# Kernel tuning notes

Measured on AMD Instinct MI355X. Metric: run time of the kernel, lower is better.

## Reference

```python
import jax, jax.numpy as jnp
import numpy as np

ALPHA = 0.2  # LeakyReLU negative slope
NEG_INF = -9e15  # matches torch -9000000000000000.0


def setup_inputs() -> dict:
    key = jax.random.key(0)
    k1, k2, k3, k4, k5, k6 = jax.random.split(key, 6)
    N, F_in, F_out = 4096, 512, 256
    adj = jax.random.randint(k1, (N, N), 0, 2, dtype=jnp.int32)
    h = jax.random.normal(k2, (N, F_in), dtype=jnp.float32)
    # proj: Linear(F_in, F_out)
    W = jax.random.normal(k3, (F_in, F_out), dtype=jnp.float32) * (1.0 / np.sqrt(F_in))
    b = jax.random.normal(k4, (F_out,), dtype=jnp.float32) * 0.01
    # proj_a: Linear(2*F_out, 1) split into the two halves acting on src/dst features
    a1 = jax.random.normal(k5, (F_out,), dtype=jnp.float32) * (1.0 / np.sqrt(2 * F_out))
    a2 = jax.random.normal(k6, (F_out,), dtype=jnp.float32) * (1.0 / np.sqrt(2 * F_out))
    a_b = jnp.zeros((), dtype=jnp.float32)
    return {"adj": adj, "h": h, "W": W, "b": b, "a1": a1, "a2": a2, "a_b": a_b}


def reference(adj, h, W, b, a1, a2, a_b):
    # wh = proj(h): [N, F_out]
    wh = h @ W + b
    # Fused form of the N x N x 2F concat + Linear(2F,1):
    # logits[i, j] = wh[i] . a1 + wh[j] . a2 + a_b
    f_src = wh @ a1  # [N]
    f_dst = wh @ a2  # [N]
    e = jax.nn.leaky_relu(f_src[:, None] + f_dst[None, :] + a_b, negative_slope=ALPHA)
    e = jnp.where(adj > 0, e, NEG_INF)
    att = jax.nn.softmax(e, axis=-1)  # F.softmax legacy dim=1 for 2D
    # dropout: inference mode (no-op) for deterministic reference
    out = att @ wh  # [N, F_out]
    return jax.nn.elu(out)  # concat=True
```

## Files before the change

### kernel.cpp

```cpp
#include <hip/hip_runtime.h>

#define NN   4096
#define FIN  512
#define FOUT 256
#define ALPHA 0.2f

typedef __attribute__((ext_vector_type(8))) short short8;
typedef __attribute__((ext_vector_type(4))) float f32x4;
typedef unsigned short u16;

__device__ __forceinline__ u16 f2bf(float x) {
    union { float f; unsigned u; } v; v.f = x;
    unsigned r = v.u + 0x7FFF + ((v.u >> 16) & 1);
    return (u16)(r >> 16);
}

__global__ __launch_bounds__(256) void k_wt(const float* __restrict__ W,
                                            u16* __restrict__ Wt,
                                            float* __restrict__ fs,
                                            float* __restrict__ fd) {
    __shared__ float s[64 * 65];
    const int t  = threadIdx.x;
    const int g  = (blockIdx.y * gridDim.x + blockIdx.x) * 256 + t;
    if (g < NN) fs[g] = 0.f; else fd[g - NN] = 0.f;
    const int f0 = blockIdx.x * 64;
    const int k0 = blockIdx.y * 64;
    #pragma unroll
    for (int p = 0; p < 4; ++p) {
        int q = t + 256 * p, rr = q >> 4, cc = q & 15;
        float4 w4 = *(const float4*)&W[(size_t)(k0 + rr) * FOUT + f0 + cc * 4];
        s[(cc * 4 + 0) * 65 + rr] = w4.x;
        s[(cc * 4 + 1) * 65 + rr] = w4.y;
        s[(cc * 4 + 2) * 65 + rr] = w4.z;
        s[(cc * 4 + 3) * 65 + rr] = w4.w;
    }
    __syncthreads();
    #pragma unroll
    for (int p = 0; p < 4; ++p) {
        int q = t + 256 * p, f = q >> 4, kg = q & 15;
        ushort4 o;
        o.x = f2bf(s[f * 65 + kg * 4 + 0]);
        o.y = f2bf(s[f * 65 + kg * 4 + 1]);
        o.z = f2bf(s[f * 65 + kg * 4 + 2]);
        o.w = f2bf(s[f * 65 + kg * 4 + 3]);
        *(ushort4*)&Wt[(size_t)(f0 + f) * FIN + k0 + kg * 4] = o;
    }
}

#define HS 520
__global__ __launch_bounds__(256) void k_proj(const float* __restrict__ h,
                                              const u16* __restrict__ Wt,
                                              const float* __restrict__ bias,
                                              const float* __restrict__ a1,
                                              const float* __restrict__ a2,
                                              u16* __restrict__ whT,
                                              float* __restrict__ fs,
                                              float* __restrict__ fd) {
    __shared__ u16 s_h[32 * HS];
    const int t  = threadIdx.x;
    const int f0 = blockIdx.x * 64;
    const int i0 = blockIdx.y * 32;
    #pragma unroll
    for (int p = 0; p < 16; ++p) {
        int q = t + 256 * p, row = q >> 7, c4 = q & 127;
        float4 v = *(const float4*)&h[(size_t)(i0 + row) * FIN + c4 * 4];
        ushort4 o; o.x = f2bf(v.x); o.y = f2bf(v.y); o.z = f2bf(v.z); o.w = f2bf(v.w);
        *(ushort4*)&s_h[row * HS + c4 * 4] = o;
    }
    __syncthreads();
    const int w = t >> 6, l = t & 63, n = l & 15, quad = l >> 4;
    const int hh = w & 1, fh = w >> 1;
    f32x4 acc[2] = {{0.f,0.f,0.f,0.f},{0.f,0.f,0.f,0.f}};
    #pragma unroll
    for (int k0 = 0; k0 < FIN; k0 += 32) {
        short8 a = *(const short8*)&s_h[(hh * 16 + n) * HS + k0 + quad * 8];
        short8 b0 = *(const short8*)&Wt[(size_t)(f0 + fh * 32 + n) * FIN + k0 + quad * 8];
        short8 b1 = *(const short8*)&Wt[(size_t)(f0 + fh * 32 + 16 + n) * FIN + k0 + quad * 8];
        acc[0] = __builtin_amdgcn_mfma_f32_16x16x32_bf16(a, b0, acc[0], 0, 0, 0);
        acc[1] = __builtin_amdgcn_mfma_f32_16x16x32_bf16(a, b1, acc[1], 0, 0, 0);
    }
    const int fb = f0 + fh * 32 + n;
    const float bv0 = bias[fb],  bv1 = bias[fb + 16];
    const float a10 = a1[fb],    a11 = a1[fb + 16];
    const float a20 = a2[fb],    a21 = a2[fb + 16];
    u16* wt_tile = whT + (size_t)(i0 >> 5) * (FOUT * 32);
    float d1[4], d2[4];
    #pragma unroll
    for (int r = 0; r < 4; ++r) {
        const int ic = hh * 16 + quad * 4 + r;
        const float v0 = acc[0][r] + bv0;
        const float v1 = acc[1][r] + bv1;
        wt_tile[fb * 32 + ic]        = f2bf(v0);
        wt_tile[(fb + 16) * 32 + ic] = f2bf(v1);
        d1[r] = v0 * a10 + v1 * a11;
        d2[r] = v0 * a20 + v1 * a21;
    }
    #pragma unroll
    for (int m = 1; m < 16; m <<= 1) {
        #pragma unroll
        for (int r = 0; r < 4; ++r) {
            d1[r] += __shfl_xor(d1[r], m);
            d2[r] += __shfl_xor(d2[r], m);
        }
    }
    if (n == 0) {
        #pragma unroll
        for (int r = 0; r < 4; ++r) {
            const int i = i0 + hh * 16 + quad * 4 + r;
            atomicAdd(&fs[i], d1[r]);
            atomicAdd(&fd[i], d2[r]);
        }
    }
}

#define BI 32
#define TJ 64
__global__ __launch_bounds__(256) void k_attn(const int* __restrict__ adj,
                                              const u16* __restrict__ whT,
                                              const float* __restrict__ fs,
                                              const float* __restrict__ fd,
                                              const float* __restrict__ ab,
                                              float* __restrict__ part,
                                              float* __restrict__ psum) {
    __shared__ u16 s_p[2][BI * 64];
    const int t  = threadIdx.x;
    const int i0 = blockIdx.x * BI;
    const int c  = blockIdx.y;
    const int jchunk = NN / gridDim.y;
    const int jbeg = c * jchunk, jend = jbeg + jchunk;
    const int jq = t & 15, rh = t >> 4;
    const float fs0 = fs[i0 + rh] + ab[0];
    const float fs1 = fs[i0 + rh + 16] + ab[0];
    const int w = t >> 6, l = t & 63, n = l & 15, quad = l >> 4;

    f32x4 acc[2][4] = {{{0.f,0.f,0.f,0.f},{0.f,0.f,0.f,0.f},{0.f,0.f,0.f,0.f},{0.f,0.f,0.f,0.f}},
                       {{0.f,0.f,0.f,0.f},{0.f,0.f,0.f,0.f},{0.f,0.f,0.f,0.f},{0.f,0.f,0.f,0.f}}};
    float rs0 = 0.f, rs1 = 0.f;

    int4   av0 = *(const int4*)&adj[(size_t)(i0 + rh) * NN + jbeg + jq * 4];
    int4   av1 = *(const int4*)&adj[(size_t)(i0 + rh + 16) * NN + jbeg + jq * 4];
    float4 fdv = *(const float4*)&fd[jbeg + jq * 4];

    const int wbase = rh * 128 + ((jq * 8) ^ ((rh & 7) << 4));
    const int rsw   = (n & 7) << 4;
    int pb = 0;
    for (int j0 = jbeg; j0 < jend; j0 += TJ) {
        short8 b[2][4];
        #pragma unroll
        for (int s = 0; s < 2; ++s) {
            const u16* tb = whT + (size_t)((j0 >> 5) + s) * (FOUT * 32) + quad * 8;
            #pragma unroll
            for (int u = 0; u < 4; ++u)
                b[s][u] = *(const short8*)&tb[(w * 64 + u * 16 + n) * 32];
        }
        ushort4 o0, o1;
        {
            float x, p;
            x = fs0 + fdv.x; x = x > 0.f ? x : ALPHA * x; p = av0.x > 0 ? __expf(x) : 0.f; o0.x = f2bf(p); rs0 += p;
            x = fs0 + fdv.y; x = x > 0.f ? x : ALPHA * x; p = av0.y > 0 ? __expf(x) : 0.f; o0.y = f2bf(p); rs0 += p;
            x = fs0 + fdv.z; x = x > 0.f ? x : ALPHA * x; p = av0.z > 0 ? __expf(x) : 0.f; o0.z = f2bf(p); rs0 += p;
            x = fs0 + fdv.w; x = x > 0.f ? x : ALPHA * x; p = av0.w > 0 ? __expf(x) : 0.f; o0.w = f2bf(p); rs0 += p;
            x = fs1 + fdv.x; x = x > 0.f ? x : ALPHA * x; p = av1.x > 0 ? __expf(x) : 0.f; o1.x = f2bf(p); rs1 += p;
            x = fs1 + fdv.y; x = x > 0.f ? x : ALPHA * x; p = av1.y > 0 ? __expf(x) : 0.f; o1.y = f2bf(p); rs1 += p;
            x = fs1 + fdv.z; x = x > 0.f ? x : ALPHA * x; p = av1.z > 0 ? __expf(x) : 0.f; o1.z = f2bf(p); rs1 += p;
            x = fs1 + fdv.w; x = x > 0.f ? x : ALPHA * x; p = av1.w > 0 ? __expf(x) : 0.f; o1.w = f2bf(p); rs1 += p;
        }
        char* spB = (char*)s_p + pb * 4096;
        *(ushort4*)(spB + wbase)        = o0;
        *(ushort4*)(spB + 2048 + wbase) = o1;
        if (j0 + TJ < jend) {
            av0 = *(const int4*)&adj[(size_t)(i0 + rh) * NN + j0 + TJ + jq * 4];
            av1 = *(const int4*)&adj[(size_t)(i0 + rh + 16) * NN + j0 + TJ + jq * 4];
            fdv = *(const float4*)&fd[j0 + TJ + jq * 4];
        }
        __syncthreads();
        __builtin_amdgcn_s_setprio(1);
        #pragma unroll
        for (int s = 0; s < 2; ++s) {
            const int rb = n * 128 + ((s * 64 + quad * 16) ^ rsw);
            short8 a0  = *(const short8*)(spB + rb);
            short8 a1f = *(const short8*)(spB + 2048 + rb);
            #pragma unroll
            for (int u = 0; u < 4; ++u) {
                acc[0][u] = __builtin_amdgcn_mfma_f32_16x16x32_bf16(a0,  b[s][u], acc[0][u], 0, 0, 0);
                acc[1][u] = __builtin_amdgcn_mfma_f32_16x16x32_bf16(a1f, b[s][u], acc[1][u], 0, 0, 0);
            }
        }
        __builtin_amdgcn_s_setprio(0);
        pb ^= 1;
    }
    #pragma unroll
    for (int m = 8; m > 0; m >>= 1) {
        rs0 += __shfl_xor(rs0, m);
        rs1 += __shfl_xor(rs1, m);
    }
    if (jq == 0) {
        psum[(size_t)c * NN + i0 + rh]      = rs0;
        psum[(size_t)c * NN + i0 + rh + 16] = rs1;
    }
    float* pc = part + ((size_t)c * NN + i0) * FOUT;
    #pragma unroll
    for (int hf = 0; hf < 2; ++hf)
        #pragma unroll
        for (int u = 0; u < 4; ++u)
            #pragma unroll
            for (int r = 0; r < 4; ++r)
                pc[(size_t)(hf * 16 + quad * 4 + r) * FOUT + w * 64 + u * 16 + n] = acc[hf][u][r];
}

__global__ __launch_bounds__(256) void k_fin(const float* __restrict__ part,
                                             const float* __restrict__ psum,
                                             float* __restrict__ out, int C) {
    const int g = blockIdx.x * 256 + threadIdx.x;
    const int i = g >> 6;
    const size_t s4 = (size_t)NN * FOUT / 4;
    float4 a = ((const float4*)part)[g];
    float s = psum[i];
    for (int c = 1; c < C; ++c) {
        float4 bb = ((const float4*)part)[g + (size_t)c * s4];
        a.x += bb.x; a.y += bb.y; a.z += bb.z; a.w += bb.w;
        s += psum[(size_t)c * NN + i];
    }
    const float inv = 1.0f / s;
    a.x *= inv; a.y *= inv; a.z *= inv; a.w *= inv;
    a.x = a.x > 0.f ? a.x : __expf(a.x) - 1.f;
    a.y = a.y > 0.f ? a.y : __expf(a.y) - 1.f;
    a.z = a.z > 0.f ? a.z : __expf(a.z) - 1.f;
    a.w = a.w > 0.f ? a.w : __expf(a.w) - 1.f;
    ((float4*)out)[g] = a;
}

extern "C" void kernel_launch(void* const* d_in, const int* in_sizes, int n_in,
                              void* d_out, int out_size, void* d_ws, size_t ws_size,
                              hipStream_t stream) {
    const int*   adj = (const int*)  d_in[0];
    const float* h   = (const float*)d_in[1];
    const float* W   = (const float*)d_in[2];
    const float* b   = (const float*)d_in[3];
    const float* a1  = (const float*)d_in[4];
    const float* a2  = (const float*)d_in[5];
    const float* ab  = (const float*)d_in[6];
    float* out = (float*)d_out;

    auto need = [](int c) -> size_t {
        size_t fl = 2 * NN + (size_t)c * NN + (size_t)c * NN * FOUT;
        size_t us = (size_t)FOUT * FIN + (size_t)NN * FOUT;
        return fl * 4 + us * 2;
    };
    int C = 4;
    while (C > 1 && need(C) > ws_size) C >>= 1;

    float* fs   = (float*)d_ws;
    float* fd   = fs + NN;
    float* psum = fd + NN;
    float* part = psum + (size_t)C * NN;
    u16*   Wt   = (u16*)(part + (size_t)C * NN * FOUT);
    u16*   whT  = Wt + (size_t)FOUT * FIN;

    k_wt  <<<dim3(FOUT / 64, FIN / 64), 256, 0, stream>>>(W, Wt, fs, fd);
    k_proj<<<dim3(FOUT / 64, NN / 32), 256, 0, stream>>>(h, Wt, b, a1, a2, whT, fs, fd);
    k_attn<<<dim3(NN / BI, C), 256, 0, stream>>>(adj, whT, fs, fd, ab, part, psum);
    k_fin <<<(NN * FOUT / 4) / 256, 256, 0, stream>>>(part, psum, out, C);
}
```

Baseline: 149.7 us.

## Factor attention exponentials per row/column and build MFMA operands in registers

The attention kernel now factors exp(leakyrelu(s_i+d_j)) into per-row and per-column exponential products. A new small kernel precomputes exp(d) and exp(alpha*d), so the inner loop needs only compares and multiplies instead of per-element exp. Each lane now computes its own bf16 A-fragment directly in registers, which removes the shared-memory staging, swizzle and __syncthreads from the loop. The j-split is fixed at 8 chunks, giving more blocks but a larger partial buffer for the final reduction. The product form can overflow or lose precision for large logits, and the fixed workspace size no longer falls back when ws_size is small.

```diff
diff --git a/kernel.cpp b/kernel.cpp
--- a/kernel.cpp
+++ b/kernel.cpp
@@ -113,90 +113,109 @@
     }
 }
 
+__global__ __launch_bounds__(256) void k_exp(const float* __restrict__ fd,
+                                             float* __restrict__ Fj,
+                                             float* __restrict__ Hj) {
+    const int g = blockIdx.x * 256 + threadIdx.x;
+    float4 v = ((const float4*)fd)[g];
+    float4 F, H;
+    F.x = __expf(v.x); F.y = __expf(v.y); F.z = __expf(v.z); F.w = __expf(v.w);
+    H.x = __expf(ALPHA * v.x); H.y = __expf(ALPHA * v.y);
+    H.z = __expf(ALPHA * v.z); H.w = __expf(ALPHA * v.w);
+    ((float4*)Fj)[g] = F;
+    ((float4*)Hj)[g] = H;
+}
+
 #define BI 32
-#define TJ 64
+#define KJ 32
+#define CJ 8
 __global__ __launch_bounds__(256) void k_attn(const int* __restrict__ adj,
                                               const u16* __restrict__ whT,
                                               const float* __restrict__ fs,
-                                              const float* __restrict__ fd,
+                                              const float* __restrict__ Fj,
+                                              const float* __restrict__ Hj,
                                               const float* __restrict__ ab,
                                               float* __restrict__ part,
                                               float* __restrict__ psum) {
-    __shared__ u16 s_p[2][BI * 64];
-    const int t  = threadIdx.x;
+    const int t = threadIdx.x;
+    const int w = t >> 6, l = t & 63, n = l & 15, quad = l >> 4;
     const int i0 = blockIdx.x * BI;
     const int c  = blockIdx.y;
-    const int jchunk = NN / gridDim.y;
-    const int jbeg = c * jchunk, jend = jbeg + jchunk;
-    const int jq = t & 15, rh = t >> 4;
-    const float fs0 = fs[i0 + rh] + ab[0];
-    const float fs1 = fs[i0 + rh + 16] + ab[0];
-    const int w = t >> 6, l = t & 63, n = l & 15, quad = l >> 4;
+    const int jbeg = c * (NN / CJ), jend = jbeg + (NN / CJ);
+    const int fw  = w * 64;
+    const int jq8 = quad * 8;
+
+    const float abv = ab[0];
+    const float s0 = fs[i0 + n] + abv;
+    const float s1 = fs[i0 + 16 + n] + abv;
+    const float E0 = __expf(s0), G0 = __expf(ALPHA * s0), R0 = __expf(-s0);
+    const float E1 = __expf(s1), G1 = __expf(ALPHA * s1), R1 = __expf(-s1);
 
     f32x4 acc[2][4] = {{{0.f,0.f,0.f,0.f},{0.f,0.f,0.f,0.f},{0.f,0.f,0.f,0.f},{0.f,0.f,0.f,0.f}},
                        {{0.f,0.f,0.f,0.f},{0.f,0.f,0.f,0.f},{0.f,0.f,0.f,0.f},{0.f,0.f,0.f,0.f}}};
     float rs0 = 0.f, rs1 = 0.f;
 
-    int4   av0 = *(const int4*)&adj[(size_t)(i0 + rh) * NN + jbeg + jq * 4];
-    int4   av1 = *(const int4*)&adj[(size_t)(i0 + rh + 16) * NN + jbeg + jq * 4];
-    float4 fdv = *(const float4*)&fd[jbeg + jq * 4];
-
-    const int wbase = rh * 128 + ((jq * 8) ^ ((rh & 7) << 4));
-    const int rsw   = (n & 7) << 4;
-    int pb = 0;
-    for (int j0 = jbeg; j0 < jend; j0 += TJ) {
-        short8 b[2][4];
-        #pragma unroll
-        for (int s = 0; s < 2; ++s) {
-            const u16* tb = whT + (size_t)((j0 >> 5) + s) * (FOUT * 32) + quad * 8;
-            #pragma unroll
-            for (int u = 0; u < 4; ++u)
-                b[s][u] = *(const short8*)&tb[(w * 64 + u * 16 + n) * 32];
-        }
-        ushort4 o0, o1;
-        {
-            float x, p;
-            x = fs0 + fdv.x; x = x > 0.f ? x : ALPHA * x; p = av0.x > 0 ? __expf(x) : 0.f; o0.x = f2bf(p); rs0 += p;
-            x = fs0 + fdv.y; x = x > 0.f ? x : ALPHA * x; p = av0.y > 0 ? __expf(x) : 0.f; o0.y = f2bf(p); rs0 += p;
-            x = fs0 + fdv.z; x = x > 0.f ? x : ALPHA * x; p = av0.z > 0 ? __expf(x) : 0.f; o0.z = f2bf(p); rs0 += p;
-            x = fs0 + fdv.w; x = x > 0.f ? x : ALPHA * x; p = av0.w > 0 ? __expf(x) : 0.f; o0.w = f2bf(p); rs0 += p;
-            x = fs1 + fdv.x; x = x > 0.f ? x : ALPHA * x; p = av1.x > 0 ? __expf(x) : 0.f; o1.x = f2bf(p); rs1 += p;
-            x = fs1 + fdv.y; x = x > 0.f ? x : ALPHA * x; p = av1.y > 0 ? __expf(x) : 0.f; o1.y = f2bf(p); rs1 += p;
-            x = fs1 + fdv.z; x = x > 0.f ? x : ALPHA * x; p = av1.z > 0 ? __expf(x) : 0.f; o1.z = f2bf(p); rs1 += p;
-            x = fs1 + fdv.w; x = x > 0.f ? x : ALPHA * x; p = av1.w > 0 ? __expf(x) : 0.f; o1.w = f2bf(p); rs1 += p;
-        }
-        char* spB = (char*)s_p + pb * 4096;
-        *(ushort4*)(spB + wbase)        = o0;
-        *(ushort4*)(spB + 2048 + wbase) = o1;
-        if (j0 + TJ < jend) {
-            av0 = *(const int4*)&adj[(size_t)(i0 + rh) * NN + j0 + TJ + jq * 4];
-            av1 = *(const int4*)&adj[(size_t)(i0 + rh + 16) * NN + j0 + TJ + jq * 4];
-            fdv = *(const float4*)&fd[j0 + TJ + jq * 4];
-        }
-        __syncthreads();
-        __builtin_amdgcn_s_setprio(1);
-        #pragma unroll
-        for (int s = 0; s < 2; ++s) {
-            const int rb = n * 128 + ((s * 64 + quad * 16) ^ rsw);
-            short8 a0  = *(const short8*)(spB + rb);
-            short8 a1f = *(const short8*)(spB + 2048 + rb);
-            #pragma unroll
-            for (int u = 0; u < 4; ++u) {
-                acc[0][u] = __builtin_amdgcn_mfma_f32_16x16x32_bf16(a0,  b[s][u], acc[0][u], 0, 0, 0);
-                acc[1][u] = __builtin_amdgcn_mfma_f32_16x16x32_bf16(a1f, b[s][u], acc[1][u], 0, 0, 0);
-            }
-        }
-        __builtin_amdgcn_s_setprio(0);
-        pb ^= 1;
-    }
-    #pragma unroll
-    for (int m = 8; m > 0; m >>= 1) {
-        rs0 += __shfl_xor(rs0, m);
-        rs1 += __shfl_xor(rs1, m);
-    }
-    if (jq == 0) {
-        psum[(size_t)c * NN + i0 + rh]      = rs0;
-        psum[(size_t)c * NN + i0 + rh + 16] = rs1;
+    const size_t ar0 = (size_t)(i0 + n) * NN;
+    const size_t ar1 = (size_t)(i0 + 16 + n) * NN;
+
+    int4 c0a = *(const int4*)&adj[ar0 + jbeg + jq8];
+    int4 c0b = *(const int4*)&adj[ar0 + jbeg + jq8 + 4];
+    int4 c1a = *(const int4*)&adj[ar1 + jbeg + jq8];
+    int4 c1b = *(const int4*)&adj[ar1 + jbeg + jq8 + 4];
+
+#define PEL(FV, HV, AV, E, G, R, OO, IDX, RS) do {            \
+        float _mi = (FV) >= (R) ? (E) : (G);                  \
+        float _mj = (FV) >= (R) ? (FV) : (HV);                \
+        float _p  = ((AV) > 0) ? _mi * _mj : 0.f;             \
+        OO.e[IDX] = f2bf(_p); RS += _p; } while (0)
+
+    #pragma unroll 2
+    for (int j0 = jbeg; j0 < jend; j0 += KJ) {
+        const u16* tb = whT + (size_t)(j0 >> 5) * (FOUT * 32) + quad * 8;
+        short8 b[4];
+        #pragma unroll
+        for (int u = 0; u < 4; ++u)
+            b[u] = *(const short8*)&tb[(fw + u * 16 + n) * 32];
+        float4 Fa = *(const float4*)&Fj[j0 + jq8];
+        float4 Fb = *(const float4*)&Fj[j0 + jq8 + 4];
+        float4 Ha = *(const float4*)&Hj[j0 + jq8];
+        float4 Hb = *(const float4*)&Hj[j0 + jq8 + 4];
+        int4 a0a = c0a, a0b = c0b, a1a = c1a, a1b = c1b;
+        if (j0 + KJ < jend) {
+            c0a = *(const int4*)&adj[ar0 + j0 + KJ + jq8];
+            c0b = *(const int4*)&adj[ar0 + j0 + KJ + jq8 + 4];
+            c1a = *(const int4*)&adj[ar1 + j0 + KJ + jq8];
+            c1b = *(const int4*)&adj[ar1 + j0 + KJ + jq8 + 4];
+        }
+        union { short8 v; u16 e[8]; } o0, o1;
+        PEL(Fa.x, Ha.x, a0a.x, E0, G0, R0, o0, 0, rs0);
+        PEL(Fa.y, Ha.y, a0a.y, E0, G0, R0, o0, 1, rs0);
+        PEL(Fa.z, Ha.z, a0a.z, E0, G0, R0, o0, 2, rs0);
+        PEL(Fa.w, Ha.w, a0a.w, E0, G0, R0, o0, 3, rs0);
+        PEL(Fb.x, Hb.x, a0b.x, E0, G0, R0, o0, 4, rs0);
+        PEL(Fb.y, Hb.y, a0b.y, E0, G0, R0, o0, 5, rs0);
+        PEL(Fb.z, Hb.z, a0b.z, E0, G0, R0, o0, 6, rs0);
+        PEL(Fb.w, Hb.w, a0b.w, E0, G0, R0, o0, 7, rs0);
+        PEL(Fa.x, Ha.x, a1a.x, E1, G1, R1, o1, 0, rs1);
+        PEL(Fa.y, Ha.y, a1a.y, E1, G1, R1, o1, 1, rs1);
+        PEL(Fa.z, Ha.z, a1a.z, E1, G1, R1, o1, 2, rs1);
+        PEL(Fa.w, Ha.w, a1a.w, E1, G1, R1, o1, 3, rs1);
+        PEL(Fb.x, Hb.x, a1b.x, E1, G1, R1, o1, 4, rs1);
+        PEL(Fb.y, Hb.y, a1b.y, E1, G1, R1, o1, 5, rs1);
+        PEL(Fb.z, Hb.z, a1b.z, E1, G1, R1, o1, 6, rs1);
+        PEL(Fb.w, Hb.w, a1b.w, E1, G1, R1, o1, 7, rs1);
+        #pragma unroll
+        for (int u = 0; u < 4; ++u) {
+            acc[0][u] = __builtin_amdgcn_mfma_f32_16x16x32_bf16(o0.v, b[u], acc[0][u], 0, 0, 0);
+            acc[1][u] = __builtin_amdgcn_mfma_f32_16x16x32_bf16(o1.v, b[u], acc[1][u], 0, 0, 0);
+        }
+    }
+#undef PEL
+    rs0 += __shfl_xor(rs0, 16); rs0 += __shfl_xor(rs0, 32);
+    rs1 += __shfl_xor(rs1, 16); rs1 += __shfl_xor(rs1, 32);
+    if (w == 0 && quad == 0) {
+        psum[(size_t)c * NN + i0 + n]      = rs0;
+        psum[(size_t)c * NN + i0 + 16 + n] = rs1;
     }
     float* pc = part + ((size_t)c * NN + i0) * FOUT;
     #pragma unroll
@@ -205,7 +224,7 @@
         for (int u = 0; u < 4; ++u)
             #pragma unroll
             for (int r = 0; r < 4; ++r)
-                pc[(size_t)(hf * 16 + quad * 4 + r) * FOUT + w * 64 + u * 16 + n] = acc[hf][u][r];
+                pc[(size_t)(hf * 16 + quad * 4 + r) * FOUT + fw + u * 16 + n] = acc[hf][u][r];
 }
 
 __global__ __launch_bounds__(256) void k_fin(const float* __restrict__ part,
@@ -242,23 +261,20 @@
     const float* ab  = (const float*)d_in[6];
     float* out = (float*)d_out;
 
-    auto need = [](int c) -> size_t {
-        size_t fl = 2 * NN + (size_t)c * NN + (size_t)c * NN * FOUT;
-        size_t us = (size_t)FOUT * FIN + (size_t)NN * FOUT;
-        return fl * 4 + us * 2;
-    };
-    int C = 4;
-    while (C > 1 && need(C) > ws_size) C >>= 1;
+    const int C = CJ;
 
     float* fs   = (float*)d_ws;
     float* fd   = fs + NN;
-    float* psum = fd + NN;
+    float* Fjv  = fd + NN;
+    float* Hjv  = Fjv + NN;
+    float* psum = Hjv + NN;
     float* part = psum + (size_t)C * NN;
     u16*   Wt   = (u16*)(part + (size_t)C * NN * FOUT);
     u16*   whT  = Wt + (size_t)FOUT * FIN;
 
     k_wt  <<<dim3(FOUT / 64, FIN / 64), 256, 0, stream>>>(W, Wt, fs, fd);
     k_proj<<<dim3(FOUT / 64, NN / 32), 256, 0, stream>>>(h, Wt, b, a1, a2, whT, fs, fd);
-    k_attn<<<dim3(NN / BI, C), 256, 0, stream>>>(adj, whT, fs, fd, ab, part, psum);
+    k_exp <<<NN / 1024, 256, 0, stream>>>(fd, Fjv, Hjv);
+    k_attn<<<dim3(NN / BI, C), 256, 0, stream>>>(adj, whT, fs, Fjv, Hjv, ab, part, psum);
     k_fin <<<(NN * FOUT / 4) / 256, 256, 0, stream>>>(part, psum, out, C);
 }
```

New measurement: 176.7 us. 18.1% more time.
